# Optimization experiments

Hardware: AMD Instinct MI355X
Metric: run time of the kernel (lower is better)

Reference implementation:

```python
import jax, jax.numpy as jnp
import numpy as np

THRESHOLD_FACTOR = 1.25
HIDDEN = 128
B, N = 4, 2048

def setup_inputs() -> dict:
    key = jax.random.key(0)
    ks = jax.random.split(key, 11)
    def lin(k, fin, fout):
        bound = 1.0 / np.sqrt(fin)
        kw, kb = jax.random.split(k)
        W = jax.random.uniform(kw, (fin, fout), jnp.float32, -bound, bound)
        b = jax.random.uniform(kb, (fout,), jnp.float32, -bound, bound)
        return W, b
    W1, b1 = lin(ks[0], 2, HIDDEN)
    W2, b2 = lin(ks[1], HIDDEN, HIDDEN)
    Wd, bd = lin(ks[2], HIDDEN, 1)
    Wr, br = lin(ks[3], HIDDEN, 1)
    Wm, bm = lin(ks[4], HIDDEN, 1)
    phase_coords = jax.random.normal(ks[5], (B, N, 2), jnp.float32)
    return dict(phase_coords=phase_coords, W1=W1, b1=b1, W2=W2, b2=b2,
                Wd=Wd, bd=bd, Wr=Wr, br=br, Wm=Wm, bm=bm)

def _attention(r):
    # diff[b,s,t,i] = r[b,s,i]*(-r[b,t,i]) + r[b,s,i] = r_s * (1 - r_t)
    diff = r[:, :, None, :] * (1.0 - r[:, None, :, :])        # [B,N,N,2]
    dist_sq = jnp.sum(diff * diff, axis=-1)                    # [B,N,N]
    phase_diff = jnp.arctan2(diff[..., 1], diff[..., 0])
    forward_bias = 0.5 * (1.0 + jnp.cos(phase_diff)) * jnp.exp(-dist_sq)
    mean_dist = jnp.mean(dist_sq, axis=(-1, -2), keepdims=True)
    std_dist = jnp.clip(jnp.std(dist_sq, axis=(-1, -2), keepdims=True, ddof=1), 1e-6, None)
    threshold = mean_dist + THRESHOLD_FACTOR * std_dist
    attn = jnp.where(dist_sq <= threshold, forward_bias, 0.0)
    row_sums = jnp.sum(attn, axis=-1, keepdims=True)
    return attn / (row_sums + 1e-8)

def reference(phase_coords, W1, b1, W2, b2, Wd, bd, Wr, br, Wm, bm):
    h = jax.nn.silu(phase_coords @ W1 + b1) @ W2 + b2           # [B,N,H]
    diffusion = h @ Wd + bd                                     # [B,N,1]
    reaction = h @ Wr + br
    migration = h @ Wm + bm
    attn = _attention(phase_coords)                             # [B,N,N]
    diffusion_field = jnp.einsum('bst,btk->bsk', attn, diffusion)
    return diffusion, reaction, migration, attn, diffusion_field
```

## Files before the change

kernel.cpp:

```cpp
#include <hip/hip_runtime.h>
#include <math.h>

#define NTOK 2048
#define HID  128
#define BB   4

typedef float f32x4 __attribute__((ext_vector_type(4)));

__device__ __forceinline__ float wave_red_f(float v) {
  #pragma unroll
  for (int o = 32; o; o >>= 1) v += __shfl_down(v, o, 64);
  return v;
}
__device__ __forceinline__ double wave_red_d(double v) {
  #pragma unroll
  for (int o = 32; o; o >>= 1) v += __shfl_down(v, o, 64);
  return v;
}

__global__ __launch_bounds__(256) void mlp_thr_kernel(
    const float* __restrict__ pc,
    const float* __restrict__ W1, const float* __restrict__ b1,
    const float* __restrict__ W2, const float* __restrict__ b2,
    const float* __restrict__ Wd, const float* __restrict__ bd,
    const float* __restrict__ Wr, const float* __restrict__ br,
    const float* __restrict__ Wm, const float* __restrict__ bm,
    float* __restrict__ outd, float* __restrict__ outr, float* __restrict__ outm,
    float* __restrict__ thr)
{
  const int tid = threadIdx.x, wave = tid >> 6, lane = tid & 63;

  if (blockIdx.x >= 256) {
    const int b = blockIdx.x - 256;
    const float2* r = (const float2*)(pc + (size_t)b * NTOK * 2);
    double m[10];
    #pragma unroll
    for (int j = 0; j < 10; ++j) m[j] = 0.0;
    for (int i = tid; i < NTOK; i += 256) {
      const float2 c = r[i];
      const double a = c.x, bq = c.y, u = 1.0 - (double)c.x, v = 1.0 - (double)c.y;
      const double a2 = a * a, b2v = bq * bq, u2 = u * u, v2 = v * v;
      m[0] += a2;       m[1] += b2v;
      m[2] += a2 * a2;  m[3] += b2v * b2v;  m[4] += a2 * b2v;
      m[5] += u2;       m[6] += v2;
      m[7] += u2 * u2;  m[8] += v2 * v2;    m[9] += u2 * v2;
    }
    #pragma unroll
    for (int j = 0; j < 10; ++j) m[j] = wave_red_d(m[j]);
    __shared__ double sm[4][10];
    if (lane == 0) {
      #pragma unroll
      for (int j = 0; j < 10; ++j) sm[wave][j] = m[j];
    }
    __syncthreads();
    if (tid == 0) {
      double t[10];
      #pragma unroll
      for (int j = 0; j < 10; ++j)
        t[j] = sm[0][j] + sm[1][j] + sm[2][j] + sm[3][j];
      const double Sq  = t[0] * t[5] + t[1] * t[6];
      const double Sqq = t[2] * t[7] + 2.0 * t[4] * t[9] + t[3] * t[8];
      const double M = (double)NTOK * (double)NTOK;
      const double mean = Sq / M;
      double var = (Sqq - Sq * Sq / M) / (M - 1.0);
      if (var < 0.0) var = 0.0;
      double sd = sqrt(var);
      if (sd < 1e-6) sd = 1e-6;
      thr[b] = (float)(mean + 1.25 * sd);
    }
    return;
  }

  __shared__ float sW2[HID * HID];
  __shared__ float sh1[4][8][HID];
  for (int i = tid; i < HID * HID; i += 256) sW2[i] = W2[i];
  __syncthreads();

  const int j0 = lane, j1 = lane + 64;
  const float w10_0 = W1[j0], w11_0 = W1[HID + j0], b1_0 = b1[j0];
  const float w10_1 = W1[j1], w11_1 = W1[HID + j1], b1_1 = b1[j1];
  const float b2_0 = b2[j0], b2_1 = b2[j1];
  const float wd0 = Wd[j0], wd1 = Wd[j1];
  const float wr0 = Wr[j0], wr1 = Wr[j1];
  const float wm0 = Wm[j0], wm1 = Wm[j1];
  const float bdv = bd[0], brv = br[0], bmv = bm[0];

  const int row0 = blockIdx.x * 32 + wave * 8;

  #pragma unroll
  for (int rr = 0; rr < 8; ++rr) {
    const float x0 = pc[(row0 + rr) * 2];
    const float x1 = pc[(row0 + rr) * 2 + 1];
    const float z0 = fmaf(x0, w10_0, fmaf(x1, w11_0, b1_0));
    const float z1 = fmaf(x0, w10_1, fmaf(x1, w11_1, b1_1));
    sh1[wave][rr][j0] = z0 / (1.f + __expf(-z0));
    sh1[wave][rr][j1] = z1 / (1.f + __expf(-z1));
  }

  float a0[8], a1[8];
  #pragma unroll
  for (int rr = 0; rr < 8; ++rr) { a0[rr] = b2_0; a1[rr] = b2_1; }
  for (int kq = 0; kq < HID / 4; ++kq) {
    float4 h[8];
    #pragma unroll
    for (int rr = 0; rr < 8; ++rr)
      h[rr] = *(const float4*)&sh1[wave][rr][kq * 4];
    #pragma unroll
    for (int i = 0; i < 4; ++i) {
      const float wA = sW2[(kq * 4 + i) * HID + j0];
      const float wB = sW2[(kq * 4 + i) * HID + j1];
      #pragma unroll
      for (int rr = 0; rr < 8; ++rr) {
        const float hv = ((const float*)&h[rr])[i];
        a0[rr] = fmaf(hv, wA, a0[rr]);
        a1[rr] = fmaf(hv, wB, a1[rr]);
      }
    }
  }

  #pragma unroll
  for (int rr = 0; rr < 8; ++rr) {
    float dd = fmaf(a0[rr], wd0, a1[rr] * wd1);
    float rv = fmaf(a0[rr], wr0, a1[rr] * wr1);
    float mv = fmaf(a0[rr], wm0, a1[rr] * wm1);
    dd = wave_red_f(dd);
    rv = wave_red_f(rv);
    mv = wave_red_f(mv);
    if (lane == 0) {
      outd[row0 + rr] = dd + bdv;
      outr[row0 + rr] = rv + brv;
      outm[row0 + rr] = mv + bmv;
    }
  }
}

__global__ __launch_bounds__(256, 6) void attn_kernel(
    const float* __restrict__ pc, const float* __restrict__ diffu,
    const float* __restrict__ thr,
    float* __restrict__ attn, float* __restrict__ dfield)
{
  const int b = blockIdx.y;
  const int tid = threadIdx.x, wave = tid >> 6, lane = tid & 63;

  const float2* __restrict__ rr  = (const float2*)(pc + (size_t)b * NTOK * 2);
  const float4* __restrict__ rr4 = (const float4*)rr;
  const float4* __restrict__ sd4 = (const float4*)(diffu + b * NTOK);

  float2 u[8];
  float  sdr[8];
  #pragma unroll
  for (int i = 0; i < 2; ++i) {
    const float4 c0 = rr4[tid * 2 + i * 512];
    const float4 c1 = rr4[tid * 2 + 1 + i * 512];
    u[i * 4 + 0] = make_float2(1.f - c0.x, 1.f - c0.y);
    u[i * 4 + 1] = make_float2(1.f - c0.z, 1.f - c0.w);
    u[i * 4 + 2] = make_float2(1.f - c1.x, 1.f - c1.y);
    u[i * 4 + 3] = make_float2(1.f - c1.z, 1.f - c1.w);
    const float4 dv = sd4[tid + i * 256];
    sdr[i * 4 + 0] = dv.x; sdr[i * 4 + 1] = dv.y;
    sdr[i * 4 + 2] = dv.z; sdr[i * 4 + 3] = dv.w;
  }

  const float T = thr[b];
  __shared__ float red[2][4][2];
  const int s0 = blockIdx.x * 4;

  for (int rs = 0; rs < 4; ++rs) {
    const int s = s0 + rs;
    const float2 rc = rr[s];
    float v[8];
    float rsum = 0.f, dot = 0.f;
    #pragma unroll
    for (int k = 0; k < 8; ++k) {
      const float d0 = rc.x * u[k].x;
      const float d1 = rc.y * u[k].y;
      const float q = fmaf(d0, d0, d1 * d1);
      float val = 0.f;
      if (q <= T)
        val = (q > 0.f) ? 0.5f * (1.f + d0 * rsqrtf(q)) * __expf(-q) : 1.f;
      v[k] = val;
      rsum += val;
      dot = fmaf(val, sdr[k], dot);
    }
    rsum = wave_red_f(rsum);
    dot  = wave_red_f(dot);
    if (lane == 0) { red[rs & 1][wave][0] = rsum; red[rs & 1][wave][1] = dot; }
    __syncthreads();
    const float rtot = red[rs & 1][0][0] + red[rs & 1][1][0] +
                       red[rs & 1][2][0] + red[rs & 1][3][0];
    const float dtot = red[rs & 1][0][1] + red[rs & 1][1][1] +
                       red[rs & 1][2][1] + red[rs & 1][3][1];
    const float sc = 1.f / (rtot + 1e-8f);
    f32x4* arow4 = (f32x4*)(attn + ((size_t)b * NTOK + s) * NTOK);
    #pragma unroll
    for (int i = 0; i < 2; ++i) {
      f32x4 o;
      o.x = v[i * 4 + 0] * sc; o.y = v[i * 4 + 1] * sc;
      o.z = v[i * 4 + 2] * sc; o.w = v[i * 4 + 3] * sc;
      __builtin_nontemporal_store(o, arow4 + tid + i * 256);
    }
    if (tid == 0) dfield[b * NTOK + s] = dtot * sc;
  }
}

extern "C" void kernel_launch(void* const* d_in, const int* in_sizes, int n_in,
                              void* d_out, int out_size, void* d_ws, size_t ws_size,
                              hipStream_t stream) {
  const float* pc = (const float*)d_in[0];
  const float* W1 = (const float*)d_in[1];
  const float* b1 = (const float*)d_in[2];
  const float* W2 = (const float*)d_in[3];
  const float* b2 = (const float*)d_in[4];
  const float* Wd = (const float*)d_in[5];
  const float* bd = (const float*)d_in[6];
  const float* Wr = (const float*)d_in[7];
  const float* br = (const float*)d_in[8];
  const float* Wm = (const float*)d_in[9];
  const float* bm = (const float*)d_in[10];

  float* out    = (float*)d_out;
  float* outd   = out;
  float* outr   = out + BB * NTOK;
  float* outm   = out + 2 * BB * NTOK;
  float* attn   = out + 3 * BB * NTOK;
  float* dfield = attn + (size_t)BB * NTOK * NTOK;

  float* thr = (float*)d_ws;

  hipLaunchKernelGGL(mlp_thr_kernel, dim3(256 + BB), dim3(256), 0, stream,
                     pc, W1, b1, W2, b2, Wd, bd, Wr, br, Wm, bm,
                     outd, outr, outm, thr);
  hipLaunchKernelGGL(attn_kernel, dim3(NTOK / 4, BB), dim3(256), 0, stream,
                     pc, outd, thr, attn, dfield);
}
```

Baseline: 35.81 us.

## Batch four attention rows per block with one barrier and exp2 prescaling

The attention kernel now computes all four rows of a block in a single pass, so the per-row barrier and wave reductions are batched behind one __syncthreads. The coordinates are prescaled by sqrt(log2 e), which lets the kernel call the native exp2 instruction without a separate multiply. The threshold is scaled to match, and the attn stores change from nontemporal to regular. The occupancy hint drops from 6 to 4 to make room for 32 live values per thread, and the W2 staging load is vectorized to float4. The cost is higher register pressure, and regular stores may pollute the cache on a write-bound kernel.

```diff
diff --git a/kernel.cpp b/kernel.cpp
--- a/kernel.cpp
+++ b/kernel.cpp
@@ -73,7 +73,8 @@
 
   __shared__ float sW2[HID * HID];
   __shared__ float sh1[4][8][HID];
-  for (int i = tid; i < HID * HID; i += 256) sW2[i] = W2[i];
+  for (int i = tid; i < HID * HID / 4; i += 256)
+    ((float4*)sW2)[i] = ((const float4*)W2)[i];
   __syncthreads();
 
   const int j0 = lane, j1 = lane + 64;
@@ -134,7 +135,7 @@
   }
 }
 
-__global__ __launch_bounds__(256, 6) void attn_kernel(
+__global__ __launch_bounds__(256, 4) void attn_kernel(
     const float* __restrict__ pc, const float* __restrict__ diffu,
     const float* __restrict__ thr,
     float* __restrict__ attn, float* __restrict__ dfield)
@@ -146,61 +147,80 @@
   const float4* __restrict__ rr4 = (const float4*)rr;
   const float4* __restrict__ sd4 = (const float4*)(diffu + b * NTOK);
 
+  const float C = 1.2011224f;
   float2 u[8];
   float  sdr[8];
   #pragma unroll
   for (int i = 0; i < 2; ++i) {
     const float4 c0 = rr4[tid * 2 + i * 512];
     const float4 c1 = rr4[tid * 2 + 1 + i * 512];
-    u[i * 4 + 0] = make_float2(1.f - c0.x, 1.f - c0.y);
-    u[i * 4 + 1] = make_float2(1.f - c0.z, 1.f - c0.w);
-    u[i * 4 + 2] = make_float2(1.f - c1.x, 1.f - c1.y);
-    u[i * 4 + 3] = make_float2(1.f - c1.z, 1.f - c1.w);
+    u[i * 4 + 0] = make_float2(C * (1.f - c0.x), C * (1.f - c0.y));
+    u[i * 4 + 1] = make_float2(C * (1.f - c0.z), C * (1.f - c0.w));
+    u[i * 4 + 2] = make_float2(C * (1.f - c1.x), C * (1.f - c1.y));
+    u[i * 4 + 3] = make_float2(C * (1.f - c1.z), C * (1.f - c1.w));
     const float4 dv = sd4[tid + i * 256];
     sdr[i * 4 + 0] = dv.x; sdr[i * 4 + 1] = dv.y;
     sdr[i * 4 + 2] = dv.z; sdr[i * 4 + 3] = dv.w;
   }
 
-  const float T = thr[b];
-  __shared__ float red[2][4][2];
+  const float Ts = thr[b] * 1.442695041f;
   const int s0 = blockIdx.x * 4;
-
-  for (int rs = 0; rs < 4; ++rs) {
-    const int s = s0 + rs;
-    const float2 rc = rr[s];
-    float v[8];
-    float rsum = 0.f, dot = 0.f;
-    #pragma unroll
-    for (int k = 0; k < 8; ++k) {
-      const float d0 = rc.x * u[k].x;
-      const float d1 = rc.y * u[k].y;
+  const float2 rc0 = rr[s0 + 0], rc1 = rr[s0 + 1];
+  const float2 rc2 = rr[s0 + 2], rc3 = rr[s0 + 3];
+
+  float v[4][8];
+  float rsum[4] = {0.f, 0.f, 0.f, 0.f};
+  float dot[4]  = {0.f, 0.f, 0.f, 0.f};
+
+  #pragma unroll
+  for (int k = 0; k < 8; ++k) {
+    const float ux = u[k].x, uy = u[k].y, dk = sdr[k];
+    #pragma unroll
+    for (int r = 0; r < 4; ++r) {
+      const float2 rc = (r == 0) ? rc0 : (r == 1) ? rc1 : (r == 2) ? rc2 : rc3;
+      const float d0 = rc.x * ux;
+      const float d1 = rc.y * uy;
       const float q = fmaf(d0, d0, d1 * d1);
       float val = 0.f;
-      if (q <= T)
-        val = (q > 0.f) ? 0.5f * (1.f + d0 * rsqrtf(q)) * __expf(-q) : 1.f;
-      v[k] = val;
-      rsum += val;
-      dot = fmaf(val, sdr[k], dot);
-    }
-    rsum = wave_red_f(rsum);
-    dot  = wave_red_f(dot);
-    if (lane == 0) { red[rs & 1][wave][0] = rsum; red[rs & 1][wave][1] = dot; }
-    __syncthreads();
-    const float rtot = red[rs & 1][0][0] + red[rs & 1][1][0] +
-                       red[rs & 1][2][0] + red[rs & 1][3][0];
-    const float dtot = red[rs & 1][0][1] + red[rs & 1][1][1] +
-                       red[rs & 1][2][1] + red[rs & 1][3][1];
-    const float sc = 1.f / (rtot + 1e-8f);
-    f32x4* arow4 = (f32x4*)(attn + ((size_t)b * NTOK + s) * NTOK);
+      if (q <= Ts)
+        val = (q > 0.f)
+            ? fmaf(d0 * rsqrtf(q), 0.5f, 0.5f) * __builtin_amdgcn_exp2f(-q)
+            : 1.f;
+      v[r][k] = val;
+      rsum[r] += val;
+      dot[r] = fmaf(val, dk, dot[r]);
+    }
+  }
+
+  __shared__ float red[4][4][2];
+  #pragma unroll
+  for (int r = 0; r < 4; ++r) {
+    rsum[r] = wave_red_f(rsum[r]);
+    dot[r]  = wave_red_f(dot[r]);
+    if (lane == 0) { red[wave][r][0] = rsum[r]; red[wave][r][1] = dot[r]; }
+  }
+  __syncthreads();
+
+  float sc[4], dtot[4];
+  #pragma unroll
+  for (int r = 0; r < 4; ++r) {
+    const float rtot = red[0][r][0] + red[1][r][0] + red[2][r][0] + red[3][r][0];
+    dtot[r] = red[0][r][1] + red[1][r][1] + red[2][r][1] + red[3][r][1];
+    sc[r] = 1.f / (rtot + 1e-8f);
+  }
+
+  #pragma unroll
+  for (int r = 0; r < 4; ++r) {
+    f32x4* arow4 = (f32x4*)(attn + ((size_t)b * NTOK + s0 + r) * NTOK);
     #pragma unroll
     for (int i = 0; i < 2; ++i) {
       f32x4 o;
-      o.x = v[i * 4 + 0] * sc; o.y = v[i * 4 + 1] * sc;
-      o.z = v[i * 4 + 2] * sc; o.w = v[i * 4 + 3] * sc;
-      __builtin_nontemporal_store(o, arow4 + tid + i * 256);
-    }
-    if (tid == 0) dfield[b * NTOK + s] = dtot * sc;
-  }
+      o.x = v[r][i * 4 + 0] * sc[r]; o.y = v[r][i * 4 + 1] * sc[r];
+      o.z = v[r][i * 4 + 2] * sc[r]; o.w = v[r][i * 4 + 3] * sc[r];
+      arow4[tid + i * 256] = o;
+    }
+  }
+  if (tid < 4) dfield[b * NTOK + s0 + tid] = dtot[tid] * sc[tid];
 }
 
 extern "C" void kernel_launch(void* const* d_in, const int* in_sizes, int n_in,
```

After: 40.15 us. 1.12x slower.

## Fold W2 into output heads and prescale coords for exp2 in attention

Applied to the files above, without the earlier changes.

The MLP kernel precomputes W2·Wd/Wr/Wm and b2·heads so each thread evaluates one token with a 128-wide dot product instead of a full 128x128 hidden layer, which cuts the MLP grid from 256 to 32 blocks. The attention kernel prescales (1-r) by sqrt(log2 e) so it can call the native exp2 without a multiply, and it scales the threshold to match. The occupancy hint on the attention kernel is also dropped. The risks are slight rounding differences from the folded weights and the rescaled comparison against the threshold.

```diff
diff --git a/kernel.cpp b/kernel.cpp
--- a/kernel.cpp
+++ b/kernel.cpp
@@ -28,10 +28,11 @@
     float* __restrict__ outd, float* __restrict__ outr, float* __restrict__ outm,
     float* __restrict__ thr)
 {
-  const int tid = threadIdx.x, wave = tid >> 6, lane = tid & 63;
-
-  if (blockIdx.x >= 256) {
-    const int b = blockIdx.x - 256;
+  const int tid = threadIdx.x;
+
+  if (blockIdx.x >= 32) {
+    const int wave = tid >> 6, lane = tid & 63;
+    const int b = blockIdx.x - 32;
     const float2* r = (const float2*)(pc + (size_t)b * NTOK * 2);
     double m[10];
     #pragma unroll
@@ -71,70 +72,55 @@
     return;
   }
 
-  __shared__ float sW2[HID * HID];
-  __shared__ float sh1[4][8][HID];
-  for (int i = tid; i < HID * HID; i += 256) sW2[i] = W2[i];
+  __shared__ float fw[3][HID];
+  __shared__ float fc[3];
+
+  for (int idx = tid; idx < 3 * HID; idx += 256) {
+    const int head = idx >> 7, k = idx & (HID - 1);
+    const float* wh = (head == 0) ? Wd : (head == 1) ? Wr : Wm;
+    const float4* w2row = (const float4*)(W2 + k * HID);
+    const float4* wh4   = (const float4*)wh;
+    float s = 0.f;
+    #pragma unroll 4
+    for (int j = 0; j < HID / 4; ++j) {
+      const float4 a = w2row[j], w = wh4[j];
+      s = fmaf(a.x, w.x, fmaf(a.y, w.y, fmaf(a.z, w.z, fmaf(a.w, w.w, s))));
+    }
+    fw[head][k] = s;
+  }
+  if (tid < 3) {
+    const float* wh = (tid == 0) ? Wd : (tid == 1) ? Wr : Wm;
+    const float bh  = (tid == 0) ? bd[0] : (tid == 1) ? br[0] : bm[0];
+    const float4* b24 = (const float4*)b2;
+    const float4* wh4 = (const float4*)wh;
+    float s = 0.f;
+    for (int j = 0; j < HID / 4; ++j) {
+      const float4 a = b24[j], w = wh4[j];
+      s = fmaf(a.x, w.x, fmaf(a.y, w.y, fmaf(a.z, w.z, fmaf(a.w, w.w, s))));
+    }
+    fc[tid] = s + bh;
+  }
   __syncthreads();
 
-  const int j0 = lane, j1 = lane + 64;
-  const float w10_0 = W1[j0], w11_0 = W1[HID + j0], b1_0 = b1[j0];
-  const float w10_1 = W1[j1], w11_1 = W1[HID + j1], b1_1 = b1[j1];
-  const float b2_0 = b2[j0], b2_1 = b2[j1];
-  const float wd0 = Wd[j0], wd1 = Wd[j1];
-  const float wr0 = Wr[j0], wr1 = Wr[j1];
-  const float wm0 = Wm[j0], wm1 = Wm[j1];
-  const float bdv = bd[0], brv = br[0], bmv = bm[0];
-
-  const int row0 = blockIdx.x * 32 + wave * 8;
-
-  #pragma unroll
-  for (int rr = 0; rr < 8; ++rr) {
-    const float x0 = pc[(row0 + rr) * 2];
-    const float x1 = pc[(row0 + rr) * 2 + 1];
-    const float z0 = fmaf(x0, w10_0, fmaf(x1, w11_0, b1_0));
-    const float z1 = fmaf(x0, w10_1, fmaf(x1, w11_1, b1_1));
-    sh1[wave][rr][j0] = z0 / (1.f + __expf(-z0));
-    sh1[wave][rr][j1] = z1 / (1.f + __expf(-z1));
-  }
-
-  float a0[8], a1[8];
-  #pragma unroll
-  for (int rr = 0; rr < 8; ++rr) { a0[rr] = b2_0; a1[rr] = b2_1; }
-  for (int kq = 0; kq < HID / 4; ++kq) {
-    float4 h[8];
-    #pragma unroll
-    for (int rr = 0; rr < 8; ++rr)
-      h[rr] = *(const float4*)&sh1[wave][rr][kq * 4];
-    #pragma unroll
-    for (int i = 0; i < 4; ++i) {
-      const float wA = sW2[(kq * 4 + i) * HID + j0];
-      const float wB = sW2[(kq * 4 + i) * HID + j1];
-      #pragma unroll
-      for (int rr = 0; rr < 8; ++rr) {
-        const float hv = ((const float*)&h[rr])[i];
-        a0[rr] = fmaf(hv, wA, a0[rr]);
-        a1[rr] = fmaf(hv, wB, a1[rr]);
-      }
-    }
-  }
-
-  #pragma unroll
-  for (int rr = 0; rr < 8; ++rr) {
-    float dd = fmaf(a0[rr], wd0, a1[rr] * wd1);
-    float rv = fmaf(a0[rr], wr0, a1[rr] * wr1);
-    float mv = fmaf(a0[rr], wm0, a1[rr] * wm1);
-    dd = wave_red_f(dd);
-    rv = wave_red_f(rv);
-    mv = wave_red_f(mv);
-    if (lane == 0) {
-      outd[row0 + rr] = dd + bdv;
-      outr[row0 + rr] = rv + brv;
-      outm[row0 + rr] = mv + bmv;
-    }
-  }
-}
-
-__global__ __launch_bounds__(256, 6) void attn_kernel(
+  const int row = blockIdx.x * 256 + tid;
+  const float2 c = ((const float2*)pc)[row];
+  const float x0 = c.x, x1 = c.y;
+
+  float dd = 0.f, rv = 0.f, mv = 0.f;
+  #pragma unroll 4
+  for (int k = 0; k < HID; ++k) {
+    const float z = fmaf(x0, W1[k], fmaf(x1, W1[HID + k], b1[k]));
+    const float h = z * __builtin_amdgcn_rcpf(1.f + __builtin_amdgcn_exp2f(-1.442695041f * z));
+    dd = fmaf(h, fw[0][k], dd);
+    rv = fmaf(h, fw[1][k], rv);
+    mv = fmaf(h, fw[2][k], mv);
+  }
+  outd[row] = dd + fc[0];
+  outr[row] = rv + fc[1];
+  outm[row] = mv + fc[2];
+}
+
+__global__ __launch_bounds__(256) void attn_kernel(
     const float* __restrict__ pc, const float* __restrict__ diffu,
     const float* __restrict__ thr,
     float* __restrict__ attn, float* __restrict__ dfield)
@@ -146,24 +132,25 @@
   const float4* __restrict__ rr4 = (const float4*)rr;
   const float4* __restrict__ sd4 = (const float4*)(diffu + b * NTOK);
 
+  const float C = 1.2011224f;
   float2 u[8];
   float  sdr[8];
   #pragma unroll
   for (int i = 0; i < 2; ++i) {
     const float4 c0 = rr4[tid * 2 + i * 512];
     const float4 c1 = rr4[tid * 2 + 1 + i * 512];
-    u[i * 4 + 0] = make_float2(1.f - c0.x, 1.f - c0.y);
-    u[i * 4 + 1] = make_float2(1.f - c0.z, 1.f - c0.w);
-    u[i * 4 + 2] = make_float2(1.f - c1.x, 1.f - c1.y);
-    u[i * 4 + 3] = make_float2(1.f - c1.z, 1.f - c1.w);
+    u[i * 4 + 0] = make_float2(C * (1.f - c0.x), C * (1.f - c0.y));
+    u[i * 4 + 1] = make_float2(C * (1.f - c0.z), C * (1.f - c0.w));
+    u[i * 4 + 2] = make_float2(C * (1.f - c1.x), C * (1.f - c1.y));
+    u[i * 4 + 3] = make_float2(C * (1.f - c1.z), C * (1.f - c1.w));
     const float4 dv = sd4[tid + i * 256];
     sdr[i * 4 + 0] = dv.x; sdr[i * 4 + 1] = dv.y;
     sdr[i * 4 + 2] = dv.z; sdr[i * 4 + 3] = dv.w;
   }
 
-  const float T = thr[b];
+  const float Ts = thr[b] * 1.442695041f;
+  const int s0 = blockIdx.x * 4;
   __shared__ float red[2][4][2];
-  const int s0 = blockIdx.x * 4;
 
   for (int rs = 0; rs < 4; ++rs) {
     const int s = s0 + rs;
@@ -176,8 +163,10 @@
       const float d1 = rc.y * u[k].y;
       const float q = fmaf(d0, d0, d1 * d1);
       float val = 0.f;
-      if (q <= T)
-        val = (q > 0.f) ? 0.5f * (1.f + d0 * rsqrtf(q)) * __expf(-q) : 1.f;
+      if (q <= Ts)
+        val = (q > 0.f)
+            ? fmaf(d0 * rsqrtf(q), 0.5f, 0.5f) * __builtin_amdgcn_exp2f(-q)
+            : 1.f;
       v[k] = val;
       rsum += val;
       dot = fmaf(val, sdr[k], dot);
@@ -227,7 +216,7 @@
 
   float* thr = (float*)d_ws;
 
-  hipLaunchKernelGGL(mlp_thr_kernel, dim3(256 + BB), dim3(256), 0, stream,
+  hipLaunchKernelGGL(mlp_thr_kernel, dim3(32 + BB), dim3(256), 0, stream,
                      pc, W1, b1, W2, b2, Wd, bd, Wr, br, Wm, bm,
                      outd, outr, outm, thr);
   hipLaunchKernelGGL(attn_kernel, dim3(NTOK / 4, BB), dim3(256), 0, stream,
```

Measured after the change: 35.10 us. 1.02x faster.
